# Kernel tuning notes

Hardware: AMD Instinct MI355X
Metric: run time of the kernel (lower is better)

The kernel has to match this reference:

```python
import jax, jax.numpy as jnp
import numpy as np
import math

B, L, H, NH = 4, 2048, 2048, 16
HD = H // NH  # head_dim = 128
ROPE_BASE = 10000.0


def rotate_half(x):
    x1, x2 = jnp.split(x, 2, axis=-1)
    return jnp.concatenate((-x2, x1), axis=-1)


def rope_cos_sin(seq_len, dim, dtype=jnp.float32):
    inv_freq = 1.0 / (ROPE_BASE ** (jnp.arange(0, dim, 2, dtype=jnp.float32) / dim))
    t = jnp.arange(seq_len, dtype=jnp.float32)
    freqs = jnp.outer(t, inv_freq)              # [L, dim/2]
    emb = jnp.concatenate((freqs, freqs), -1)   # [L, dim]
    return jnp.cos(emb).astype(dtype), jnp.sin(emb).astype(dtype)


def setup_inputs() -> dict:
    key = jax.random.key(0)
    ks = jax.random.split(key, 5)
    x = jax.random.normal(ks[0], (B, L, H), dtype=jnp.float32)
    # causal mask, broadcastable over [B, NH, L, L]; 0 -> masked
    mask = jnp.tril(jnp.ones((L, L), dtype=jnp.int32))[None, None]
    s = 0.02
    Wq = jax.random.normal(ks[1], (H, H), dtype=jnp.float32) * s
    Wk = jax.random.normal(ks[2], (H, H), dtype=jnp.float32) * s
    Wv = jax.random.normal(ks[3], (H, H), dtype=jnp.float32) * s
    Wo = jax.random.normal(ks[4], (H, H), dtype=jnp.float32) * s
    return {"x": x, "mask": mask, "Wq": Wq, "Wk": Wk, "Wv": Wv, "Wo": Wo}


def reference(x, mask, Wq, Wk, Wv, Wo):
    b, l, _ = x.shape
    # nn.Linear: y = x @ W.T (weight shape [out, in])
    q = (x @ Wq.T).reshape(b, l, NH, HD).transpose(0, 2, 1, 3)  # [B,H,L,D]
    k = (x @ Wk.T).reshape(b, l, NH, HD).transpose(0, 2, 1, 3)
    v = (x @ Wv.T).reshape(b, l, NH, HD).transpose(0, 2, 1, 3)
    cos, sin = rope_cos_sin(l, HD, x.dtype)  # [L, D] broadcasts over [B,H,L,D]
    q = q * cos + rotate_half(q) * sin
    k = k * cos + rotate_half(k) * sin
    attn = jnp.einsum("bhqd,bhkd->bhqk", q, k) / math.sqrt(HD)
    attn = jnp.where(mask == 0, jnp.float32(-jnp.inf), attn)
    attn = jax.nn.softmax(attn.astype(jnp.float32), axis=-1).astype(x.dtype)
    out = jnp.einsum("bhqk,bhkd->bhqd", attn, v)
    out = out.transpose(0, 2, 1, 3).reshape(b, l, NH * HD)
    return out @ Wo.T
```

## Files before the change

kernel.cpp:

```cpp
#include <hip/hip_runtime.h>
#include <cstdint>
#include <cmath>

#define B_   4
#define L_   2048
#define H_   2048
#define NH_  16
#define HD_  128
#define ML_  (B_*L_)

using short8 = __attribute__((ext_vector_type(8))) short;
using f32x4  = __attribute__((ext_vector_type(4))) float;
using f32x16 = __attribute__((ext_vector_type(16))) float;
using uint4v = __attribute__((ext_vector_type(4))) unsigned;

__device__ inline short f2bf(float f){
  unsigned u = __builtin_bit_cast(unsigned, f);
  unsigned r = u + 0x7FFFu + ((u >> 16) & 1u);
  return (short)(r >> 16);
}
__device__ inline float bf2f(short s){
  unsigned u = ((unsigned)(unsigned short)s) << 16;
  return __builtin_bit_cast(float, u);
}

#define GLD16(gp, lp) __builtin_amdgcn_global_load_lds(                      \
    (const __attribute__((address_space(1))) void*)(gp),                     \
    (__attribute__((address_space(3))) void*)(lp), 16, 0, 0)

__device__ inline unsigned cvtpk_bf16(float lo, float hi){
  unsigned d;
  asm("v_cvt_pk_bf16_f32 %0, %1, %2" : "=v"(d) : "v"(lo), "v"(hi));
  return d;
}
__device__ inline void permswap32(unsigned &a, unsigned &b){
  asm volatile("v_permlane32_swap_b32 %0, %1" : "+v"(a), "+v"(b));
}
__device__ inline float cross_half_max(float x){
  return fmaxf(x, __shfl_xor(x, 32));
}
__device__ inline float cross_half_add(float x){
  return x + __shfl_xor(x, 32);
}

__global__ void rope_table(float* __restrict__ cosT, float* __restrict__ sinT){
  int idx = blockIdx.x * 256 + threadIdx.x;
  if (idx >= L_ * 64) return;
  int l = idx >> 6, d = idx & 63;
  float invf = powf(10000.0f, -(float)d * (1.0f/64.0f));
  float fr = (float)l * invf;
  cosT[idx] = cosf(fr);
  sinT[idx] = sinf(fr);
}

__global__ __launch_bounds__(256)
void cvt_bf16(const float* __restrict__ in, short* __restrict__ out, int n8){
  int i = blockIdx.x * 256 + threadIdx.x;
  if (i >= n8) return;
  const float4* p = (const float4*)(in + (size_t)i * 8);
  float4 a = p[0], b = p[1];
  short8 s;
  s[0]=f2bf(a.x); s[1]=f2bf(a.y); s[2]=f2bf(a.z); s[3]=f2bf(a.w);
  s[4]=f2bf(b.x); s[5]=f2bf(b.y); s[6]=f2bf(b.z); s[7]=f2bf(b.w);
  *(short8*)(out + (size_t)i * 8) = s;
}

template<int OUT_F32>
__global__ __launch_bounds__(256)
void gemm_bt_bf16(const short* __restrict__ A, const short* __restrict__ Bw,
                  void* __restrict__ Cp, int M, int N, int K)
{
  __shared__ short sA[128 * 64];
  __shared__ short sB[128 * 64];
  const int tid  = threadIdx.x;
  const int lane = tid & 63;
  const int wave = tid >> 6;
  const int wr = wave >> 1, wc = wave & 1;
  const int ln = lane & 15, g = lane >> 4;

  int flat = blockIdx.y * gridDim.x + blockIdx.x;
  int wg   = (flat & 7) * 128 + (flat >> 3);
  const int m0 = (wg >> 4) * 128, n0 = (wg & 15) * 128;

  const int lrow = lane >> 3;
  const int lc4  = (lane & 7) ^ lrow;

  f32x4 acc[4][4];
  #pragma unroll
  for (int i = 0; i < 4; i++)
    #pragma unroll
    for (int j = 0; j < 4; j++) acc[i][j] = {0.f, 0.f, 0.f, 0.f};

  for (int k0 = 0; k0 < K; k0 += 64) {
    #pragma unroll
    for (int i = 0; i < 4; i++) {
      int u = wave * 4 + i;
      const short* ga = A  + (size_t)(m0 + u * 8 + lrow) * K + k0 + lc4 * 8;
      GLD16(ga, sA + u * 512);
      const short* gb = Bw + (size_t)(n0 + u * 8 + lrow) * K + k0 + lc4 * 8;
      GLD16(gb, sB + u * 512);
    }
    __syncthreads();

    #pragma unroll
    for (int kk = 0; kk < 64; kk += 32) {
      short8 af[4], bfr[4];
      #pragma unroll
      for (int m = 0; m < 4; m++) {
        int row  = wr * 64 + m * 16 + ln;
        int slot = ((kk >> 3) + g) ^ (ln & 7);
        af[m] = *(const short8*)(sA + row * 64 + slot * 8);
      }
      #pragma unroll
      for (int n = 0; n < 4; n++) {
        int row  = wc * 64 + n * 16 + ln;
        int slot = ((kk >> 3) + g) ^ (ln & 7);
        bfr[n] = *(const short8*)(sB + row * 64 + slot * 8);
      }
      #pragma unroll
      for (int m = 0; m < 4; m++)
        #pragma unroll
        for (int n = 0; n < 4; n++)
          acc[m][n] = __builtin_amdgcn_mfma_f32_16x16x32_bf16(af[m], bfr[n], acc[m][n], 0, 0, 0);
    }
    __syncthreads();
  }

  #pragma unroll
  for (int m = 0; m < 4; m++)
    #pragma unroll
    for (int n = 0; n < 4; n++)
      #pragma unroll
      for (int r = 0; r < 4; r++) {
        int row = m0 + wr * 64 + m * 16 + g * 4 + r;
        int col = n0 + wc * 64 + n * 16 + ln;
        float v = acc[m][n][r];
        if constexpr (OUT_F32) ((float*)Cp)[(size_t)row * N + col] = v;
        else                   ((short*)Cp)[(size_t)row * N + col] = f2bf(v);
      }
}

__global__ __launch_bounds__(256)
void rope_apply(short* __restrict__ Qb, short* __restrict__ Kb,
                const float* __restrict__ cosT, const float* __restrict__ sinT)
{
  int idx = blockIdx.x * 256 + threadIdx.x;
  int z = blockIdx.y;
  short* ptr  = z ? Kb : Qb;
  float scale = z ? 1.0f : 0.08838834764831845f;
  int row = idx >> 7;
  int rem = idx & 127;
  int h = rem >> 3, ch = rem & 7;
  int l = row & (L_ - 1);
  short* base = ptr + (size_t)row * H_ + h * HD_ + ch * 8;
  short8 lo = *(short8*)base;
  short8 hi = *(short8*)(base + 64);
  const float* cp = cosT + l * 64 + ch * 8;
  const float* sp = sinT + l * 64 + ch * 8;
  short8 nlo, nhi;
  #pragma unroll
  for (int j = 0; j < 8; j++) {
    float c = cp[j], s = sp[j];
    float x0 = bf2f(lo[j]), x1 = bf2f(hi[j]);
    nlo[j] = f2bf((x0 * c - x1 * s) * scale);
    nhi[j] = f2bf((x1 * c + x0 * s) * scale);
  }
  *(short8*)base        = nlo;
  *(short8*)(base + 64) = nhi;
}

__global__ __launch_bounds__(256)
void transpose_v(const short* __restrict__ Vb, short* __restrict__ VT)
{
  __shared__ short t[64 * 64];
  const int blk = blockIdx.x;
  const int dt = blk & 1, lt = (blk >> 1) & 31, bh = blk >> 6;
  const int b = bh >> 4, h = bh & 15;
  const int l0 = lt * 64, d0 = dt * 64;
  const int tid = threadIdx.x;
  #pragma unroll
  for (int i = 0; i < 2; i++) {
    int u = tid + i * 256;
    int r = u >> 3, c = u & 7;
    short8 v = *(const short8*)(Vb + ((size_t)b * L_ + l0 + r) * H_ + h * HD_ + d0 + c * 8);
    *(short8*)&t[r * 64 + ((c ^ ((r >> 3) & 7)) << 3)] = v;
  }
  __syncthreads();
  #pragma unroll
  for (int i = 0; i < 2; i++) {
    int u = tid + i * 256;
    int d = u >> 3, lc = u & 7;
    short8 o;
    #pragma unroll
    for (int j = 0; j < 8; j++) {
      int l = lc * 8 + j;
      o[j] = t[l * 64 + (((d >> 3) ^ (lc & 7)) << 3) + (d & 7)];
    }
    *(short8*)(VT + ((size_t)bh * HD_ + d0 + d) * L_ + l0 + lc * 8) = o;
  }
}

__global__ __launch_bounds__(512, 2)
void flash_attn(const short* __restrict__ Qb, const short* __restrict__ Kb,
                const short* __restrict__ VT, short* __restrict__ AO)
{
  __shared__ short lds_k[2][64 * 128];
  __shared__ short lds_v[2][128 * 64];
  __shared__ float f_lds[8][32];

  const int blk = blockIdx.x;
  int bh, j;
  if (blk < 256) { bh = blk & 63; j = 7 - (blk >> 6); }
  else           { int u = blk - 256; bh = u & 63; j = 3 - (u >> 6); }
  const int q0 = j * 256;
  const int T  = 4 * j + 4;
  const int h = bh & 15, b = bh >> 4;
  const int tid = threadIdx.x, wave = tid >> 6, lane = tid & 63;
  const int hi = lane >> 5, l31 = lane & 31;
  const size_t rowbase = (size_t)b * L_;
  const int colbase = h * HD_;
  const short* Kbh  = Kb + rowbase * H_ + colbase;
  const short* VTbh = VT + (size_t)bh * HD_ * L_;
  const int qw = q0 + wave * 32;
  const int qabs = qw + l31;

  short8 qf[8];
  {
    const short* qp = Qb + (rowbase + qabs) * H_ + colbase + hi * 8;
    #pragma unroll
    for (int c = 0; c < 8; c++) qf[c] = *(const short8*)(qp + c * 16);
  }

  f32x16 acc_o[4];
  #pragma unroll
  for (int d = 0; d < 4; d++)
    #pragma unroll
    for (int r = 0; r < 16; r++) acc_o[d][r] = 0.f;
  float m_ = -__builtin_inff(), l_ = 0.f;

  auto stage = [&](int k0s, int bufi) {
    #pragma unroll
    for (int i = 0; i < 2; i++) {
      int c = wave * 2 + i;
      {
        int grow = k0s + c * 4 + (lane >> 4);
        const short* gp = Kbh + (size_t)grow * H_ + (((lane & 15) ^ (grow & 7)) * 8);
        GLD16(gp, &lds_k[bufi][c * 512]);
      }
      {
        int d = c * 8 + (lane >> 3);
        const short* gp = VTbh + (size_t)d * L_ + k0s + (((lane & 7) ^ (d & 7)) * 8);
        GLD16(gp, &lds_v[bufi][c * 512]);
      }
    }
  };

  stage(0, 0);
  __syncthreads();

  for (int t = 0; t < T; ++t) {
    const int k0 = t * 64;
    if (t + 1 < T) stage((t + 1) * 64, (t + 1) & 1);
    const short* kb_ = lds_k[t & 1];
    const short* vb_ = lds_v[t & 1];

    if (k0 <= qw + 31) {
      f32x16 p0, p1;
      #pragma unroll
      for (int r = 0; r < 16; r++) { p0[r] = 0.f; p1[r] = 0.f; }
      __builtin_amdgcn_s_setprio(1);
      #pragma unroll
      for (int c = 0; c < 8; c++) {
        int ch = (c * 2 + hi) ^ (l31 & 7);
        short8 kf0 = *(const short8*)(kb_ + l31 * 128 + ch * 8);
        short8 kf1 = *(const short8*)(kb_ + (32 + l31) * 128 + ch * 8);
        p0 = __builtin_amdgcn_mfma_f32_32x32x16_bf16(kf0, qf[c], p0, 0, 0, 0);
        p1 = __builtin_amdgcn_mfma_f32_32x32x16_bf16(kf1, qf[c], p1, 0, 0, 0);
      }
      __builtin_amdgcn_s_setprio(0);

      if (k0 + 63 > qw) {
        #pragma unroll
        for (int r = 0; r < 16; r++) {
          int kvl = (r & 3) + 8 * (r >> 2) + 4 * hi;
          if (k0 + kvl > qabs)      p0[r] = -__builtin_inff();
          if (k0 + 32 + kvl > qabs) p1[r] = -__builtin_inff();
        }
      }

      float mt = p0[0];
      #pragma unroll
      for (int r = 1; r < 16; r++) mt = fmaxf(mt, p0[r]);
      #pragma unroll
      for (int r = 0; r < 16; r++) mt = fmaxf(mt, p1[r]);
      mt = cross_half_max(mt);
      float mnew = fmaxf(m_, mt);
      float f = __expf(m_ - mnew);
      m_ = mnew;
      float ls = 0.f;
      #pragma unroll
      for (int r = 0; r < 16; r++) { p0[r] = __expf(p0[r] - mnew); ls += p0[r]; }
      #pragma unroll
      for (int r = 0; r < 16; r++) { p1[r] = __expf(p1[r] - mnew); ls += p1[r]; }
      ls = cross_half_add(ls);
      l_ = l_ * f + ls;

      if (lane < 32) f_lds[wave][lane] = f;
      f32x4 fr[4];
      #pragma unroll
      for (int i = 0; i < 4; i++)
        fr[i] = *(const f32x4*)&f_lds[wave][i * 8 + hi * 4];
      #pragma unroll
      for (int d = 0; d < 4; d++)
        #pragma unroll
        for (int r = 0; r < 16; r++) acc_o[d][r] *= fr[r >> 2][r & 3];

      __builtin_amdgcn_s_setprio(1);
      #pragma unroll
      for (int ks = 0; ks < 4; ks++) {
        const f32x16 &pp = (ks < 2) ? p0 : p1;
        const int kk = (ks & 1) * 8;
        unsigned a0 = cvtpk_bf16(pp[kk + 0], pp[kk + 1]);
        unsigned b0 = cvtpk_bf16(pp[kk + 4], pp[kk + 5]);
        permswap32(a0, b0);
        unsigned a1 = cvtpk_bf16(pp[kk + 2], pp[kk + 3]);
        unsigned b1 = cvtpk_bf16(pp[kk + 6], pp[kk + 7]);
        permswap32(a1, b1);
        uint4v w; w[0] = a0; w[1] = a1; w[2] = b0; w[3] = b1;
        short8 af = __builtin_bit_cast(short8, w);
        #pragma unroll
        for (int db = 0; db < 4; db++) {
          int d  = db * 32 + l31;
          int ch = (ks * 2 + hi) ^ (d & 7);
          short8 vf = *(const short8*)(vb_ + d * 64 + ch * 8);
          acc_o[db] = __builtin_amdgcn_mfma_f32_32x32x16_bf16(af, vf, acc_o[db], 0, 0, 0);
        }
      }
      __builtin_amdgcn_s_setprio(0);
    }
    __syncthreads();
  }

  if (lane < 32) f_lds[wave][lane] = 1.0f / l_;
  f32x4 lr[4];
  #pragma unroll
  for (int i = 0; i < 4; i++)
    lr[i] = *(const f32x4*)&f_lds[wave][i * 8 + hi * 4];
  #pragma unroll
  for (int db = 0; db < 4; db++)
    #pragma unroll
    for (int r = 0; r < 16; r++) {
      int row = qw + (r & 3) + 8 * (r >> 2) + 4 * hi;
      AO[(rowbase + row) * H_ + colbase + db * 32 + l31] =
          f2bf(acc_o[db][r] * lr[r >> 2][r & 3]);
    }
}

extern "C" void kernel_launch(void* const* d_in, const int* in_sizes, int n_in,
                              void* d_out, int out_size, void* d_ws, size_t ws_size,
                              hipStream_t stream)
{
  const float* x  = (const float*)d_in[0];
  const float* Wq = (const float*)d_in[2];
  const float* Wk = (const float*)d_in[3];
  const float* Wv = (const float*)d_in[4];
  const float* Wo = (const float*)d_in[5];
  float* out = (float*)d_out;

  char* ws = (char*)d_ws;
  const size_t SZ = (size_t)ML_ * H_ * sizeof(short);
  short* Qb = (short*)(ws);
  short* Kb = (short*)(ws + SZ);
  short* Vb = (short*)(ws + 2 * SZ);
  short* xb = (short*)(ws + 3 * SZ);
  short* VT = xb;
  short* AO = Vb;
  short* Wb = (short*)(ws + 4 * SZ);
  float* cosT = (float*)(ws + 4 * SZ + (size_t)H_ * H_ * sizeof(short));
  float* sinT = cosT + (size_t)L_ * 64;

  rope_table<<<512, 256, 0, stream>>>(cosT, sinT);

  cvt_bf16<<<ML_ * H_ / 8 / 256, 256, 0, stream>>>(x, xb, ML_ * H_ / 8);

  dim3 gg(H_ / 128, ML_ / 128);
  cvt_bf16<<<H_ * H_ / 8 / 256, 256, 0, stream>>>(Wq, Wb, H_ * H_ / 8);
  gemm_bt_bf16<0><<<gg, 256, 0, stream>>>(xb, Wb, Qb, ML_, H_, H_);
  cvt_bf16<<<H_ * H_ / 8 / 256, 256, 0, stream>>>(Wk, Wb, H_ * H_ / 8);
  gemm_bt_bf16<0><<<gg, 256, 0, stream>>>(xb, Wb, Kb, ML_, H_, H_);
  cvt_bf16<<<H_ * H_ / 8 / 256, 256, 0, stream>>>(Wv, Wb, H_ * H_ / 8);
  gemm_bt_bf16<0><<<gg, 256, 0, stream>>>(xb, Wb, Vb, ML_, H_, H_);

  transpose_v<<<64 * 32 * 2, 256, 0, stream>>>(Vb, VT);

  rope_apply<<<dim3(ML_ * NH_ * 8 / 256, 2), 256, 0, stream>>>(Qb, Kb, cosT, sinT);

  flash_attn<<<512, 512, 0, stream>>>(Qb, Kb, VT, AO);

  cvt_bf16<<<H_ * H_ / 8 / 256, 256, 0, stream>>>(Wo, Wb, H_ * H_ / 8);
  gemm_bt_bf16<1><<<gg, 256, 0, stream>>>(AO, Wb, out, ML_, H_, H_);
}
```

Before: 537.1 us.

## Replace GEMM with 256x256 tile kernel using 4-stage LDS prefetch pipeline

```diff
diff --git a/kernel.cpp b/kernel.cpp
--- a/kernel.cpp
+++ b/kernel.cpp
@@ -66,73 +66,83 @@
 }
 
 template<int OUT_F32>
-__global__ __launch_bounds__(256)
-void gemm_bt_bf16(const short* __restrict__ A, const short* __restrict__ Bw,
-                  void* __restrict__ Cp, int M, int N, int K)
+__global__ __launch_bounds__(512, 2)
+void gemm256_bt(const short* __restrict__ A, const short* __restrict__ Bw,
+                void* __restrict__ Cp)
 {
-  __shared__ short sA[128 * 64];
-  __shared__ short sB[128 * 64];
+  constexpr int K = 2048, N = 2048;
+  __shared__ short sA[4][256 * 32];
+  __shared__ short sB[4][256 * 32];
   const int tid  = threadIdx.x;
   const int lane = tid & 63;
   const int wave = tid >> 6;
-  const int wr = wave >> 1, wc = wave & 1;
+  const int wr = wave >> 2, wc = wave & 3;
   const int ln = lane & 15, g = lane >> 4;
 
-  int flat = blockIdx.y * gridDim.x + blockIdx.x;
-  int wg   = (flat & 7) * 128 + (flat >> 3);
-  const int m0 = (wg >> 4) * 128, n0 = (wg & 15) * 128;
-
-  const int lrow = lane >> 3;
-  const int lc4  = (lane & 7) ^ lrow;
-
-  f32x4 acc[4][4];
-  #pragma unroll
-  for (int i = 0; i < 4; i++)
-    #pragma unroll
-    for (int j = 0; j < 4; j++) acc[i][j] = {0.f, 0.f, 0.f, 0.f};
-
-  for (int k0 = 0; k0 < K; k0 += 64) {
-    #pragma unroll
-    for (int i = 0; i < 4; i++) {
-      int u = wave * 4 + i;
-      const short* ga = A  + (size_t)(m0 + u * 8 + lrow) * K + k0 + lc4 * 8;
-      GLD16(ga, sA + u * 512);
-      const short* gb = Bw + (size_t)(n0 + u * 8 + lrow) * K + k0 + lc4 * 8;
-      GLD16(gb, sB + u * 512);
-    }
-    __syncthreads();
-
-    #pragma unroll
-    for (int kk = 0; kk < 64; kk += 32) {
-      short8 af[4], bfr[4];
-      #pragma unroll
-      for (int m = 0; m < 4; m++) {
-        int row  = wr * 64 + m * 16 + ln;
-        int slot = ((kk >> 3) + g) ^ (ln & 7);
-        af[m] = *(const short8*)(sA + row * 64 + slot * 8);
-      }
-      #pragma unroll
-      for (int n = 0; n < 4; n++) {
-        int row  = wc * 64 + n * 16 + ln;
-        int slot = ((kk >> 3) + g) ^ (ln & 7);
-        bfr[n] = *(const short8*)(sB + row * 64 + slot * 8);
-      }
-      #pragma unroll
-      for (int m = 0; m < 4; m++)
-        #pragma unroll
-        for (int n = 0; n < 4; n++)
-          acc[m][n] = __builtin_amdgcn_mfma_f32_16x16x32_bf16(af[m], bfr[n], acc[m][n], 0, 0, 0);
-    }
-    __syncthreads();
-  }
-
-  #pragma unroll
-  for (int m = 0; m < 4; m++)
+  const int blk = blockIdx.x;
+  const int m0 = (blk >> 3) * 256, n0 = (blk & 7) * 256;
+
+  const int u0 = wave * 64 + lane;
+  const int u1 = u0 + 512;
+  const int r0 = u0 >> 2, c0 = ((u0 & 3) ^ (r0 & 3)) * 8;
+  const int r1 = u1 >> 2, c1 = ((u1 & 3) ^ (r1 & 3)) * 8;
+
+  f32x4 acc[8][4];
+  #pragma unroll
+  for (int m = 0; m < 8; m++)
+    #pragma unroll
+    for (int n = 0; n < 4; n++) acc[m][n] = {0.f, 0.f, 0.f, 0.f};
+
+#define STAGE256(T) do {                                                     \
+    const int _b = (T) & 3; const int _k = (T) * 32;                         \
+    GLD16(A  + (size_t)(m0 + r0) * K + _k + c0, &sA[_b][wave * 512]);        \
+    GLD16(A  + (size_t)(m0 + r1) * K + _k + c1, &sA[_b][4096 + wave * 512]); \
+    GLD16(Bw + (size_t)(n0 + r0) * K + _k + c0, &sB[_b][wave * 512]);        \
+    GLD16(Bw + (size_t)(n0 + r1) * K + _k + c1, &sB[_b][4096 + wave * 512]); \
+  } while (0)
+
+#define TILE256(T, VMN, PF) do {                                             \
+    asm volatile("s_waitcnt vmcnt(" #VMN ")" ::: "memory");                  \
+    __builtin_amdgcn_s_barrier();                                            \
+    asm volatile("" ::: "memory");                                           \
+    const short* _at = &sA[(T) & 3][0];                                      \
+    const short* _bt = &sB[(T) & 3][0];                                      \
+    short8 af[8], bfr[4];                                                    \
+    const int _sl = (g ^ (ln & 3)) * 8;                                      \
+    _Pragma("unroll")                                                        \
+    for (int m = 0; m < 8; m++)                                              \
+      af[m] = *(const short8*)(_at + (wr * 128 + m * 16 + ln) * 32 + _sl);   \
+    _Pragma("unroll")                                                        \
+    for (int n = 0; n < 4; n++)                                              \
+      bfr[n] = *(const short8*)(_bt + (wc * 64 + n * 16 + ln) * 32 + _sl);   \
+    if (PF) STAGE256((T) + 3);                                               \
+    __builtin_amdgcn_s_setprio(1);                                           \
+    _Pragma("unroll")                                                        \
+    for (int m = 0; m < 8; m++)                                              \
+      _Pragma("unroll")                                                      \
+      for (int n = 0; n < 4; n++)                                            \
+        acc[m][n] = __builtin_amdgcn_mfma_f32_16x16x32_bf16(af[m], bfr[n],   \
+                                                            acc[m][n], 0, 0, 0); \
+    __builtin_amdgcn_s_setprio(0);                                           \
+  } while (0)
+
+  STAGE256(0); STAGE256(1); STAGE256(2);
+
+  for (int t = 0; t < 61; ++t) TILE256(t, 8, true);
+  TILE256(61, 8, false);
+  TILE256(62, 4, false);
+  TILE256(63, 0, false);
+
+#undef STAGE256
+#undef TILE256
+
+  #pragma unroll
+  for (int m = 0; m < 8; m++)
     #pragma unroll
     for (int n = 0; n < 4; n++)
       #pragma unroll
       for (int r = 0; r < 4; r++) {
-        int row = m0 + wr * 64 + m * 16 + g * 4 + r;
+        int row = m0 + wr * 128 + m * 16 + g * 4 + r;
         int col = n0 + wc * 64 + n * 16 + ln;
         float v = acc[m][n][r];
         if constexpr (OUT_F32) ((float*)Cp)[(size_t)row * N + col] = v;
@@ -383,13 +393,12 @@
 
   cvt_bf16<<<ML_ * H_ / 8 / 256, 256, 0, stream>>>(x, xb, ML_ * H_ / 8);
 
-  dim3 gg(H_ / 128, ML_ / 128);
   cvt_bf16<<<H_ * H_ / 8 / 256, 256, 0, stream>>>(Wq, Wb, H_ * H_ / 8);
-  gemm_bt_bf16<0><<<gg, 256, 0, stream>>>(xb, Wb, Qb, ML_, H_, H_);
+  gemm256_bt<0><<<256, 512, 0, stream>>>(xb, Wb, Qb);
   cvt_bf16<<<H_ * H_ / 8 / 256, 256, 0, stream>>>(Wk, Wb, H_ * H_ / 8);
-  gemm_bt_bf16<0><<<gg, 256, 0, stream>>>(xb, Wb, Kb, ML_, H_, H_);
+  gemm256_bt<0><<<256, 512, 0, stream>>>(xb, Wb, Kb);
   cvt_bf16<<<H_ * H_ / 8 / 256, 256, 0, stream>>>(Wv, Wb, H_ * H_ / 8);
-  gemm_bt_bf16<0><<<gg, 256, 0, stream>>>(xb, Wb, Vb, ML_, H_, H_);
+  gemm256_bt<0><<<256, 512, 0, stream>>>(xb, Wb, Vb);
 
   transpose_v<<<64 * 32 * 2, 256, 0, stream>>>(Vb, VT);
 
@@ -398,5 +407,5 @@
   flash_attn<<<512, 512, 0, stream>>>(Qb, Kb, VT, AO);
 
   cvt_bf16<<<H_ * H_ / 8 / 256, 256, 0, stream>>>(Wo, Wb, H_ * H_ / 8);
-  gemm_bt_bf16<1><<<gg, 256, 0, stream>>>(AO, Wb, out, ML_, H_, H_);
-}
+  gemm256_bt<1><<<256, 512, 0, stream>>>(AO, Wb, out);
+}
```

Result: faster. 462.1 us (-14.0%).
